# Kernel optimization log

Measured on AMD Instinct MI355X. Metric: run time of the kernel, lower is better.

Reference implementation:

```python
import jax, jax.numpy as jnp
import numpy as np

B, S, E, U, V = 64, 1024, 1024, 1024, 32000

def setup_inputs() -> dict:
    key = jax.random.key(0)
    ks = jax.random.split(key, 12)
    s = lambda fan_in: 1.0 / np.sqrt(fan_in)
    return {
        "sentence": jax.random.randint(ks[0], (B, S), 0, V, dtype=jnp.int64),
        "emb": jax.random.normal(ks[1], (V, E), jnp.float32),
        "Wf": jax.random.normal(ks[2], (E, U), jnp.float32) * s(E),
        "bf": jnp.zeros((U,), jnp.float32),
        "Wi": jax.random.normal(ks[3], (E, U), jnp.float32) * s(E),
        "bi": jnp.zeros((U,), jnp.float32),
        "Wh": jax.random.normal(ks[4], (E, U), jnp.float32) * s(E),
        "bh": jnp.zeros((U,), jnp.float32),
        "W1": jax.random.normal(ks[5], (U, 64), jnp.float32) * s(U),
        "b1": jnp.zeros((64,), jnp.float32),
        "W2": jax.random.normal(ks[6], (64, 1), jnp.float32) * s(64),
        "b2": jnp.zeros((1,), jnp.float32),
    }

def reference(sentence, emb, Wf, bf, Wi, bi, Wh, bh, W1, b1, W2, b2):
    x = emb[sentence]                                   # [B,S,E]
    # minLSTM gates depend only on x -> hoist GEMMs out of the time loop
    f = jax.nn.sigmoid(jnp.einsum('bse,eu->bsu', x, Wf) + bf)
    i = jax.nn.sigmoid(jnp.einsum('bse,eu->bsu', x, Wi) + bi)
    h_tilde = jnp.einsum('bse,eu->bsu', x, Wh) + bh
    denom = f + i
    f_n = f / denom                                     # normalized forget gate
    i_n = i / denom                                     # normalized input gate

    def step(h, gates):
        f_t, ih_t = gates                               # [B,U] each
        h = f_t * h + ih_t
        return h, None

    h0 = jnp.zeros((sentence.shape[0], Wf.shape[1]), x.dtype)
    # scan over time; precombine i_n * h_tilde
    gates = (jnp.swapaxes(f_n, 0, 1), jnp.swapaxes(i_n * h_tilde, 0, 1))  # [S,B,U]
    h, _ = jax.lax.scan(step, h0, gates)
    z = h @ W1 + b1
    z = z @ W2 + b2
    return jax.nn.sigmoid(z)                            # [B,1]
```

## Files before the change

kernel.cpp:

```cpp
#include <hip/hip_runtime.h>
#include <cstdint>

typedef unsigned short u16;
typedef __attribute__((ext_vector_type(8))) short short8;
typedef __attribute__((ext_vector_type(8))) unsigned short ushort8;
typedef __attribute__((ext_vector_type(4))) float floatx4;
typedef __attribute__((ext_vector_type(4))) _Float16 half4;

#define S_LEN 1024
#define BATCH 64
#define EDIM 1024
#define UDIM 1024
#define VOCAB 32000
#define NTOT (3 * UDIM)
#define CT 64
#define NC (S_LEN / CT)

__device__ __forceinline__ u16 f2bf(float x) {
  unsigned u = __float_as_uint(x);
  return (u16)((u + 0x7fffu + ((u >> 16) & 1u)) >> 16);
}

__device__ __forceinline__ void async16(const u16* g, u16* s) {
  __builtin_amdgcn_global_load_lds(
      (__attribute__((address_space(1))) void*)(uintptr_t)g,
      (__attribute__((address_space(3))) void*)(uintptr_t)s,
      16, 0, 0);
}

__device__ __forceinline__ float sigm(float x) {
  return __builtin_amdgcn_rcpf(1.f + __expf(-x));
}

__global__ __launch_bounds__(256) void conv_emb(const float4* __restrict__ in,
                                                ushort4* __restrict__ out, long n4) {
  long i = (long)blockIdx.x * 256 + threadIdx.x;
  if (i >= n4) return;
  float4 v = in[i];
  ushort4 o;
  o.x = f2bf(v.x); o.y = f2bf(v.y); o.z = f2bf(v.z); o.w = f2bf(v.w);
  out[i] = o;
}

__global__ __launch_bounds__(256) void conv_wt(const float* __restrict__ Wf,
                                               const float* __restrict__ Wi,
                                               const float* __restrict__ Wh,
                                               u16* __restrict__ wtB) {
  __shared__ float t[32][33];
  const float* W = (blockIdx.z == 0) ? Wf : ((blockIdx.z == 1) ? Wi : Wh);
  int bx = blockIdx.x * 32;
  int by = blockIdx.y * 32;
  int tx = threadIdx.x, ty = threadIdx.y;
  for (int j = 0; j < 32; j += 8)
    t[ty + j][tx] = W[(size_t)(by + ty + j) * UDIM + bx + tx];
  __syncthreads();
  u16* out = wtB + (size_t)blockIdx.z * UDIM * EDIM;
  for (int j = 0; j < 32; j += 8)
    out[(size_t)(bx + ty + j) * EDIM + by + tx] = f2bf(t[tx][ty + j]);
}

__global__ __launch_bounds__(256, 3) void gate_gemm(
    const u16* __restrict__ embB, const u16* __restrict__ wtB,
    const float* __restrict__ bfp, const float* __restrict__ bip,
    const float* __restrict__ bhp,
    u16* __restrict__ FnT, u16* __restrict__ GT) {
  __shared__ __align__(16) u16 As[128 * 64];
  __shared__ __align__(16) u16 Bs[192 * 64];

  const int tid = threadIdx.x;
  const int wave = tid >> 6;
  const int lane = tid & 63;

  const int g = blockIdx.x;
  const int x = g & 7;
  const int s = g >> 3;
  const int mtile = s >> 1;
  const int utile = x * 2 + (s & 1);
  const int m0 = mtile * 128;
  const int u0 = utile * 64;

  const u16* gA[4]; int loA[4];
  const u16* gB[6]; int loB[6];
#pragma unroll
  for (int j = 0; j < 4; ++j) {
    int idx = j * 256 + tid;
    int r = idx >> 3;
    int cg = (idx & 7) ^ (r & 7);
    gA[j] = embB + (size_t)(m0 + r) * EDIM + cg * 8;
    loA[j] = idx * 8;
  }
#pragma unroll
  for (int j = 0; j < 6; ++j) {
    int idx = j * 256 + tid;
    int r = idx >> 3;
    int gr = (r >> 6) * UDIM + u0 + (r & 63);
    int cg = (idx & 7) ^ (r & 7);
    gB[j] = wtB + (size_t)gr * EDIM + cg * 8;
    loB[j] = idx * 8;
  }

  floatx4 acc[8][3] = {};
  const int fr = lane & 15;
  const int fq = lane >> 4;
  const int fr7 = fr & 7;
  const int un = wave * 16 + fr;

  for (int k0 = 0; k0 < EDIM; k0 += 64) {
#pragma unroll
    for (int j = 0; j < 4; ++j) async16(gA[j] + k0, &As[loA[j]]);
#pragma unroll
    for (int j = 0; j < 6; ++j) async16(gB[j] + k0, &Bs[loB[j]]);
    __syncthreads();
#pragma unroll
    for (int kk = 0; kk < 2; ++kk) {
      const int swz = ((kk * 4 + fq) ^ fr7) * 8;
      short8 b0 = *(const short8*)&Bs[(0 * 64 + un) * 64 + swz];
      short8 b1 = *(const short8*)&Bs[(1 * 64 + un) * 64 + swz];
      short8 b2 = *(const short8*)&Bs[(2 * 64 + un) * 64 + swz];
#pragma unroll
      for (int mt = 0; mt < 8; ++mt) {
        short8 am = *(const short8*)&As[(mt * 16 + fr) * 64 + swz];
        acc[mt][0] = __builtin_amdgcn_mfma_f32_16x16x32_bf16(am, b0, acc[mt][0], 0, 0, 0);
        acc[mt][1] = __builtin_amdgcn_mfma_f32_16x16x32_bf16(am, b1, acc[mt][1], 0, 0, 0);
        acc[mt][2] = __builtin_amdgcn_mfma_f32_16x16x32_bf16(am, b2, acc[mt][2], 0, 0, 0);
      }
    }
    __syncthreads();
  }

  const int ug = u0 + un;
  const float bfv = bfp[ug], biv = bip[ug], bhv = bhp[ug];
  u16* outF = As;
  u16* outG = Bs;
#pragma unroll
  for (int mt = 0; mt < 8; ++mt) {
#pragma unroll
    for (int r = 0; r < 4; ++r) {
      float fs = sigm(acc[mt][0][r] + bfv);
      float is = sigm(acc[mt][1][r] + biv);
      float hv = acc[mt][2][r] + bhv;
      float inv = __builtin_amdgcn_rcpf(fs + is);
      float fn = fs * inv;
      float gv = is * inv * hv;
      int row = mt * 16 + fq * 4 + r;
      outF[row * 64 + un] = __builtin_bit_cast(u16, (_Float16)fn);
      outG[row * 64 + un] = __builtin_bit_cast(u16, (_Float16)gv);
    }
  }
  __syncthreads();
#pragma unroll
  for (int j = 0; j < 4; ++j) {
    int idx = j * 256 + tid;
    int row = idx >> 3, cc = idx & 7;
    size_t gb = (size_t)(m0 + row) * UDIM + u0 + cc * 8;
    *(ushort8*)&FnT[gb] = *(const ushort8*)&outF[idx * 8];
    *(ushort8*)&GT[gb] = *(const ushort8*)&outG[idx * 8];
  }
}

__global__ __launch_bounds__(256) void scan_gather(
    const int* __restrict__ sent, const u16* __restrict__ FnT,
    const u16* __restrict__ GT, float* __restrict__ Fc, float* __restrict__ Gc) {
  const int b = blockIdx.x >> 4;
  const int c = blockIdx.x & (NC - 1);
  const int tid = threadIdx.x;
  __shared__ int toks[CT];
  if (tid < CT) toks[tid] = sent[b * S_LEN + c * CT + tid];
  __syncthreads();
  const int uo = tid * 4;
  floatx4 F = {1.f, 1.f, 1.f, 1.f};
  floatx4 G = {0.f, 0.f, 0.f, 0.f};
#pragma unroll 8
  for (int t = 0; t < CT; ++t) {
    const size_t ro = (size_t)toks[t] * UDIM + uo;
    ushort4 fraw = *(const ushort4*)&FnT[ro];
    ushort4 graw = *(const ushort4*)&GT[ro];
    half4 fh = __builtin_bit_cast(half4, fraw);
    half4 gh = __builtin_bit_cast(half4, graw);
    floatx4 fn = {(float)fh.x, (float)fh.y, (float)fh.z, (float)fh.w};
    floatx4 gv = {(float)gh.x, (float)gh.y, (float)gh.z, (float)gh.w};
    G = fn * G + gv;
    F = F * fn;
  }
  const size_t o = (size_t)c * (BATCH * UDIM) + (size_t)b * UDIM + uo;
  *(floatx4*)&Fc[o] = F;
  *(floatx4*)&Gc[o] = G;
}

__global__ __launch_bounds__(256) void mlp_head(
    const float* __restrict__ Fc, const float* __restrict__ Gc,
    const float* __restrict__ W1, const float* __restrict__ b1,
    const float* __restrict__ W2, const float* __restrict__ b2,
    float* __restrict__ out) {
  const int b = blockIdx.x;
  const int tid = threadIdx.x;
  __shared__ float h_s[UDIM];
  __shared__ float z1[64];
  for (int u = tid; u < UDIM; u += 256) {
    float h = 0.f;
#pragma unroll
    for (int c = 0; c < NC; ++c) {
      float F = Fc[c * (BATCH * UDIM) + b * UDIM + u];
      float G = Gc[c * (BATCH * UDIM) + b * UDIM + u];
      h = F * h + G;
    }
    h_s[u] = h;
  }
  __syncthreads();
  const int j = tid >> 2, p = tid & 3;
  float partial = 0.f;
  for (int u = p * 256; u < p * 256 + 256; ++u) partial += h_s[u] * W1[u * 64 + j];
  partial += __shfl_down(partial, 1);
  partial += __shfl_down(partial, 2);
  if (p == 0) z1[j] = partial + b1[j];
  __syncthreads();
  if (tid < 64) {
    float v = z1[tid] * W2[tid];
#pragma unroll
    for (int off = 32; off > 0; off >>= 1) v += __shfl_down(v, off);
    if (tid == 0) out[b] = 1.f / (1.f + __expf(-(v + b2[0])));
  }
}

extern "C" void kernel_launch(void* const* d_in, const int* in_sizes, int n_in,
                              void* d_out, int out_size, void* d_ws, size_t ws_size,
                              hipStream_t stream) {
  const int* sent = (const int*)d_in[0];
  const float* emb = (const float*)d_in[1];
  const float* Wf = (const float*)d_in[2];
  const float* bf_ = (const float*)d_in[3];
  const float* Wi = (const float*)d_in[4];
  const float* bi_ = (const float*)d_in[5];
  const float* Wh = (const float*)d_in[6];
  const float* bh_ = (const float*)d_in[7];
  const float* W1 = (const float*)d_in[8];
  const float* b1 = (const float*)d_in[9];
  const float* W2 = (const float*)d_in[10];
  const float* b2 = (const float*)d_in[11];
  float* out = (float*)d_out;

  char* ws = (char*)d_ws;
  u16* embB = (u16*)ws;   ws += (size_t)VOCAB * EDIM * 2;
  u16* wtB = (u16*)ws;    ws += (size_t)NTOT * EDIM * 2;
  u16* FnT = (u16*)ws;    ws += (size_t)VOCAB * UDIM * 2;
  u16* GT = (u16*)ws;     ws += (size_t)VOCAB * UDIM * 2;
  float* Fc = (float*)ws; ws += (size_t)NC * BATCH * UDIM * 4;
  float* Gc = (float*)ws; ws += (size_t)NC * BATCH * UDIM * 4;

  long n4 = (long)VOCAB * EDIM / 4;
  hipLaunchKernelGGL(conv_emb, dim3((unsigned)(n4 / 256)), dim3(256), 0, stream,
                     (const float4*)emb, (ushort4*)embB, n4);
  hipLaunchKernelGGL(conv_wt, dim3(32, 32, 3), dim3(32, 8), 0, stream, Wf, Wi, Wh, wtB);
  hipLaunchKernelGGL(gate_gemm, dim3((VOCAB / 128) * (NTOT / 192)), dim3(256), 0, stream,
                     embB, wtB, bf_, bi_, bh_, FnT, GT);
  hipLaunchKernelGGL(scan_gather, dim3(BATCH * NC), dim3(256), 0, stream,
                     sent, FnT, GT, Fc, Gc);
  hipLaunchKernelGGL(mlp_head, dim3(BATCH), dim3(256), 0, stream, Fc, Gc, W1, b1, W2, b2, out);
}
```

Measured before the change: 461.5 us.

## Fuse embedding bf16 conversion into gate GEMM and interleave F/G table

Removes the separate conv_emb pass that wrote a bf16 copy of the whole embedding table. The gate GEMM now loads fp32 embedding rows directly into registers, packs them to bf16 with v_cvt_pk_bf16_f32 and stores them to LDS. The F and G outputs are also interleaved into one table, so the scan gather fetches both with a single 16-byte load. The cost is that the A-operand path becomes synchronous register loads instead of async global-to-LDS copies, and the GEMM now reads twice as many A bytes from global memory. Each A tile row is reread by every u-tile block.

```diff
diff --git a/kernel.cpp b/kernel.cpp
--- a/kernel.cpp
+++ b/kernel.cpp
@@ -5,7 +5,8 @@
 typedef __attribute__((ext_vector_type(8))) short short8;
 typedef __attribute__((ext_vector_type(8))) unsigned short ushort8;
 typedef __attribute__((ext_vector_type(4))) float floatx4;
-typedef __attribute__((ext_vector_type(4))) _Float16 half4;
+typedef __attribute__((ext_vector_type(8))) _Float16 half8;
+typedef __attribute__((ext_vector_type(4))) unsigned uintx4;
 
 #define S_LEN 1024
 #define BATCH 64
@@ -21,6 +22,12 @@
   return (u16)((u + 0x7fffu + ((u >> 16) & 1u)) >> 16);
 }
 
+__device__ __forceinline__ unsigned pk_bf16(float a, float b) {
+  unsigned r;
+  asm("v_cvt_pk_bf16_f32 %0, %1, %2" : "=v"(r) : "v"(a), "v"(b));
+  return r;
+}
+
 __device__ __forceinline__ void async16(const u16* g, u16* s) {
   __builtin_amdgcn_global_load_lds(
       (__attribute__((address_space(1))) void*)(uintptr_t)g,
@@ -30,16 +37,6 @@
 
 __device__ __forceinline__ float sigm(float x) {
   return __builtin_amdgcn_rcpf(1.f + __expf(-x));
-}
-
-__global__ __launch_bounds__(256) void conv_emb(const float4* __restrict__ in,
-                                                ushort4* __restrict__ out, long n4) {
-  long i = (long)blockIdx.x * 256 + threadIdx.x;
-  if (i >= n4) return;
-  float4 v = in[i];
-  ushort4 o;
-  o.x = f2bf(v.x); o.y = f2bf(v.y); o.z = f2bf(v.z); o.w = f2bf(v.w);
-  out[i] = o;
 }
 
 __global__ __launch_bounds__(256) void conv_wt(const float* __restrict__ Wf,
@@ -60,12 +57,12 @@
 }
 
 __global__ __launch_bounds__(256, 3) void gate_gemm(
-    const u16* __restrict__ embB, const u16* __restrict__ wtB,
+    const float* __restrict__ emb, const u16* __restrict__ wtB,
     const float* __restrict__ bfp, const float* __restrict__ bip,
-    const float* __restrict__ bhp,
-    u16* __restrict__ FnT, u16* __restrict__ GT) {
-  __shared__ __align__(16) u16 As[128 * 64];
-  __shared__ __align__(16) u16 Bs[192 * 64];
+    const float* __restrict__ bhp, u16* __restrict__ FG) {
+  __shared__ __align__(16) u16 SM[128 * 64 + 192 * 64];
+  u16* As = SM;
+  u16* Bs = SM + 128 * 64;
 
   const int tid = threadIdx.x;
   const int wave = tid >> 6;
@@ -79,14 +76,14 @@
   const int m0 = mtile * 128;
   const int u0 = utile * 64;
 
-  const u16* gA[4]; int loA[4];
+  const float* gAf[4]; int loA[4];
   const u16* gB[6]; int loB[6];
 #pragma unroll
   for (int j = 0; j < 4; ++j) {
     int idx = j * 256 + tid;
     int r = idx >> 3;
     int cg = (idx & 7) ^ (r & 7);
-    gA[j] = embB + (size_t)(m0 + r) * EDIM + cg * 8;
+    gAf[j] = emb + (size_t)(m0 + r) * EDIM + cg * 8;
     loA[j] = idx * 8;
   }
 #pragma unroll
@@ -107,9 +104,22 @@
 
   for (int k0 = 0; k0 < EDIM; k0 += 64) {
 #pragma unroll
-    for (int j = 0; j < 4; ++j) async16(gA[j] + k0, &As[loA[j]]);
-#pragma unroll
     for (int j = 0; j < 6; ++j) async16(gB[j] + k0, &Bs[loB[j]]);
+    float4 fa[8];
+#pragma unroll
+    for (int j = 0; j < 4; ++j) {
+      fa[2 * j] = *(const float4*)(gAf[j] + k0);
+      fa[2 * j + 1] = *(const float4*)(gAf[j] + k0 + 4);
+    }
+#pragma unroll
+    for (int j = 0; j < 4; ++j) {
+      uintx4 p;
+      p.x = pk_bf16(fa[2 * j].x, fa[2 * j].y);
+      p.y = pk_bf16(fa[2 * j].z, fa[2 * j].w);
+      p.z = pk_bf16(fa[2 * j + 1].x, fa[2 * j + 1].y);
+      p.w = pk_bf16(fa[2 * j + 1].z, fa[2 * j + 1].w);
+      *(short8*)&As[loA[j]] = __builtin_bit_cast(short8, p);
+    }
     __syncthreads();
 #pragma unroll
     for (int kk = 0; kk < 2; ++kk) {
@@ -130,8 +140,8 @@
 
   const int ug = u0 + un;
   const float bfv = bfp[ug], biv = bip[ug], bhv = bhp[ug];
-  u16* outF = As;
-  u16* outG = Bs;
+  u16* FGs = SM;
+  const int up = un ^ ((fq & 1) << 4);
 #pragma unroll
   for (int mt = 0; mt < 8; ++mt) {
 #pragma unroll
@@ -143,46 +153,44 @@
       float fn = fs * inv;
       float gv = is * inv * hv;
       int row = mt * 16 + fq * 4 + r;
-      outF[row * 64 + un] = __builtin_bit_cast(u16, (_Float16)fn);
-      outG[row * 64 + un] = __builtin_bit_cast(u16, (_Float16)gv);
-    }
-  }
-  __syncthreads();
-#pragma unroll
-  for (int j = 0; j < 4; ++j) {
+      unsigned pkfg = (unsigned)__builtin_bit_cast(u16, (_Float16)fn) |
+                      ((unsigned)__builtin_bit_cast(u16, (_Float16)gv) << 16);
+      *(unsigned*)&FGs[row * 128 + up * 2] = pkfg;
+    }
+  }
+  __syncthreads();
+#pragma unroll
+  for (int j = 0; j < 8; ++j) {
     int idx = j * 256 + tid;
-    int row = idx >> 3, cc = idx & 7;
-    size_t gb = (size_t)(m0 + row) * UDIM + u0 + cc * 8;
-    *(ushort8*)&FnT[gb] = *(const ushort8*)&outF[idx * 8];
-    *(ushort8*)&GT[gb] = *(const ushort8*)&outG[idx * 8];
+    int row = idx >> 4, cc = idx & 15;
+    int ccp = cc ^ (((row >> 2) & 1) << 2);
+    *(ushort8*)&FG[(size_t)(m0 + row) * (2 * UDIM) + u0 * 2 + cc * 8] =
+        *(const ushort8*)&FGs[row * 128 + ccp * 8];
   }
 }
 
 __global__ __launch_bounds__(256) void scan_gather(
-    const int* __restrict__ sent, const u16* __restrict__ FnT,
-    const u16* __restrict__ GT, float* __restrict__ Fc, float* __restrict__ Gc) {
+    const int* __restrict__ sent, const u16* __restrict__ FG,
+    float* __restrict__ Fc, float* __restrict__ Gc) {
   const int b = blockIdx.x >> 4;
   const int c = blockIdx.x & (NC - 1);
   const int tid = threadIdx.x;
   __shared__ int toks[CT];
   if (tid < CT) toks[tid] = sent[b * S_LEN + c * CT + tid];
   __syncthreads();
-  const int uo = tid * 4;
+  const int uo2 = tid * 8;
   floatx4 F = {1.f, 1.f, 1.f, 1.f};
   floatx4 G = {0.f, 0.f, 0.f, 0.f};
 #pragma unroll 8
   for (int t = 0; t < CT; ++t) {
-    const size_t ro = (size_t)toks[t] * UDIM + uo;
-    ushort4 fraw = *(const ushort4*)&FnT[ro];
-    ushort4 graw = *(const ushort4*)&GT[ro];
-    half4 fh = __builtin_bit_cast(half4, fraw);
-    half4 gh = __builtin_bit_cast(half4, graw);
-    floatx4 fn = {(float)fh.x, (float)fh.y, (float)fh.z, (float)fh.w};
-    floatx4 gv = {(float)gh.x, (float)gh.y, (float)gh.z, (float)gh.w};
+    const size_t ro = (size_t)toks[t] * (2 * UDIM) + uo2;
+    half8 fg = __builtin_bit_cast(half8, *(const ushort8*)&FG[ro]);
+    floatx4 fn = {(float)fg[0], (float)fg[2], (float)fg[4], (float)fg[6]};
+    floatx4 gv = {(float)fg[1], (float)fg[3], (float)fg[5], (float)fg[7]};
     G = fn * G + gv;
     F = F * fn;
   }
-  const size_t o = (size_t)c * (BATCH * UDIM) + (size_t)b * UDIM + uo;
+  const size_t o = (size_t)c * (BATCH * UDIM) + (size_t)b * UDIM + tid * 4;
   *(floatx4*)&Fc[o] = F;
   *(floatx4*)&Gc[o] = G;
 }
@@ -240,20 +248,15 @@
   float* out = (float*)d_out;
 
   char* ws = (char*)d_ws;
-  u16* embB = (u16*)ws;   ws += (size_t)VOCAB * EDIM * 2;
   u16* wtB = (u16*)ws;    ws += (size_t)NTOT * EDIM * 2;
-  u16* FnT = (u16*)ws;    ws += (size_t)VOCAB * UDIM * 2;
-  u16* GT = (u16*)ws;     ws += (size_t)VOCAB * UDIM * 2;
+  u16* FG = (u16*)ws;     ws += (size_t)VOCAB * UDIM * 2 * 2;
   float* Fc = (float*)ws; ws += (size_t)NC * BATCH * UDIM * 4;
   float* Gc = (float*)ws; ws += (size_t)NC * BATCH * UDIM * 4;
 
-  long n4 = (long)VOCAB * EDIM / 4;
-  hipLaunchKernelGGL(conv_emb, dim3((unsigned)(n4 / 256)), dim3(256), 0, stream,
-                     (const float4*)emb, (ushort4*)embB, n4);
   hipLaunchKernelGGL(conv_wt, dim3(32, 32, 3), dim3(32, 8), 0, stream, Wf, Wi, Wh, wtB);
   hipLaunchKernelGGL(gate_gemm, dim3((VOCAB / 128) * (NTOT / 192)), dim3(256), 0, stream,
-                     embB, wtB, bf_, bi_, bh_, FnT, GT);
+                     emb, wtB, bf_, bi_, bh_, FG);
   hipLaunchKernelGGL(scan_gather, dim3(BATCH * NC), dim3(256), 0, stream,
-                     sent, FnT, GT, Fc, Gc);
+                     sent, FG, Fc, Gc);
   hipLaunchKernelGGL(mlp_head, dim3(BATCH), dim3(256), 0, stream, Fc, Gc, W1, b1, W2, b2, out);
 }
```

Result: slower. 517.2 us (+12.1%).
